# Kernel optimization log

Measured on AMD Instinct MI355X. Metric: run time of the kernel, lower is better.

Reference implementation:

```python
import jax, jax.numpy as jnp
import numpy as np

COMMITMENT_COST = 0.25
ENTROPY_WEIGHT = 0.1
EPS = 1e-10


def setup_inputs() -> dict:
    key = jax.random.key(0)
    k1, k2 = jax.random.split(key)
    B, L, D, K = 8, 4096, 256, 4096
    z = jax.random.normal(k1, (B, L, D), dtype=jnp.float32)
    # torch init: uniform(-1/K, 1/K)
    codebook_weight = jax.random.uniform(k2, (K, D), dtype=jnp.float32,
                                         minval=-1.0 / K, maxval=1.0 / K)
    return {"z": z, "codebook_weight": codebook_weight}


def reference(z, codebook_weight):
    B, L, D = z.shape
    z_flat = z.reshape(-1, D)                       # [N, D]
    # squared euclidean distances: [N, K]
    d2 = (jnp.sum(z_flat ** 2, axis=1, keepdims=True)
          + jnp.sum(codebook_weight ** 2, axis=1)
          - 2.0 * z_flat @ codebook_weight.T)
    indices = jnp.argmin(d2, axis=1)                # [N]
    z_q_flat = codebook_weight[indices]             # gather [N, D]
    z_q = z_q_flat.reshape(B, L, D)

    codebook_loss = jnp.mean((z_q - jax.lax.stop_gradient(z)) ** 2)
    commitment_loss = jnp.mean((jax.lax.stop_gradient(z_q) - z) ** 2)

    probs = jax.nn.softmax(-d2, axis=1)             # [N, K]
    avg_probs = probs.mean(axis=0)                  # [K]
    entropy = -jnp.sum(avg_probs * jnp.log(avg_probs + EPS))
    entropy_loss = -entropy

    codebook_commitment_loss = codebook_loss + COMMITMENT_COST * commitment_loss
    scaled_entropy_loss = ENTROPY_WEIGHT * entropy_loss
    vq_loss = codebook_commitment_loss + scaled_entropy_loss

    # straight-through estimator
    z_q_ste = z + jax.lax.stop_gradient(z_q - z)
    indices_out = indices.reshape(B, L)
    return (z_q_ste, indices_out, vq_loss, codebook_commitment_loss, scaled_entropy_loss)
```

## Files before the change

kernel.cpp:

```cpp
#include <hip/hip_runtime.h>
#include <stdint.h>

#define NROWS 32768
#define KC 4096
#define DIM 256
#define BM 64
#define TPS 64
#define CAP 40
#define KAPPA 0.99960f
#define K2L2E 2.88539008f
#define L2E 1.44269504f

#define OUT_IDX (NROWS * DIM)
#define OUT_SCAL (OUT_IDX + NROWS)

#define WS_CNORM 0
#define WS_ZNORM 16384
#define WS_LOSS  147456
#define WS_AVGP8 147712
#define WS_FRAG  278784

typedef __bf16 bf8 __attribute__((ext_vector_type(8)));
typedef float f16v __attribute__((ext_vector_type(16)));

#define GLOAD_LDS(g, l) \
  __builtin_amdgcn_global_load_lds( \
      (const __attribute__((address_space(1))) void*)(g), \
      (__attribute__((address_space(3))) void*)(l), 16, 0, 0)

__device__ __forceinline__ unsigned ford(float f) {
  unsigned u = __float_as_uint(f);
  return (u & 0x80000000u) ? ~u : (u | 0x80000000u);
}

__device__ __forceinline__ float np_rownorm256(const float* __restrict__ p) {
  float h[2];
  #pragma unroll
  for (int half = 0; half < 2; ++half) {
    const float* b = p + half * 128;
    float r[8];
    {
      float4 v0 = *(const float4*)(b);
      float4 v1 = *(const float4*)(b + 4);
      r[0] = __fmul_rn(v0.x, v0.x); r[1] = __fmul_rn(v0.y, v0.y);
      r[2] = __fmul_rn(v0.z, v0.z); r[3] = __fmul_rn(v0.w, v0.w);
      r[4] = __fmul_rn(v1.x, v1.x); r[5] = __fmul_rn(v1.y, v1.y);
      r[6] = __fmul_rn(v1.z, v1.z); r[7] = __fmul_rn(v1.w, v1.w);
    }
    for (int i = 8; i < 128; i += 8) {
      float4 v0 = *(const float4*)(b + i);
      float4 v1 = *(const float4*)(b + i + 4);
      r[0] = __fadd_rn(r[0], __fmul_rn(v0.x, v0.x));
      r[1] = __fadd_rn(r[1], __fmul_rn(v0.y, v0.y));
      r[2] = __fadd_rn(r[2], __fmul_rn(v0.z, v0.z));
      r[3] = __fadd_rn(r[3], __fmul_rn(v0.w, v0.w));
      r[4] = __fadd_rn(r[4], __fmul_rn(v1.x, v1.x));
      r[5] = __fadd_rn(r[5], __fmul_rn(v1.y, v1.y));
      r[6] = __fadd_rn(r[6], __fmul_rn(v1.z, v1.z));
      r[7] = __fadd_rn(r[7], __fmul_rn(v1.w, v1.w));
    }
    h[half] = __fadd_rn(
        __fadd_rn(__fadd_rn(r[0], r[1]), __fadd_rn(r[2], r[3])),
        __fadd_rn(__fadd_rn(r[4], r[5]), __fadd_rn(r[6], r[7])));
  }
  return __fadd_rn(h[0], h[1]);
}

__global__ void k_norms(const float* __restrict__ cbw, const float* __restrict__ z,
                        float* __restrict__ cnorm, float* __restrict__ znorm) {
  int r = blockIdx.x * 256 + threadIdx.x;
  if (r < KC) cnorm[r] = np_rownorm256(cbw + (size_t)r * DIM);
  else {
    int q = r - KC;
    if (q < NROWS) znorm[q] = np_rownorm256(z + (size_t)q * DIM);
  }
}

__global__ void k_frag(const float* __restrict__ cbw, __bf16* __restrict__ frag) {
  int idx = blockIdx.x * 256 + threadIdx.x;
  int c = idx >> 5, u = idx & 31;
  int ds = u >> 1, half = u & 1;
  int ct = c >> 5, m = c & 31;
  int lane = half * 32 + m;
  const float* src = cbw + (size_t)c * DIM + ds * 16 + half * 8;
  float4 a = *(const float4*)src;
  float4 b = *(const float4*)(src + 4);
  bf8 h;
  h[0] = (__bf16)a.x; h[1] = (__bf16)a.y; h[2] = (__bf16)a.z; h[3] = (__bf16)a.w;
  h[4] = (__bf16)b.x; h[5] = (__bf16)b.y; h[6] = (__bf16)b.z; h[7] = (__bf16)b.w;
  *(bf8*)(frag + ((size_t)(ct * 16 + ds) * 64 + lane) * 8) = h;
}

__device__ __forceinline__ float exact_d2(const float* __restrict__ zr,
                                          const float* __restrict__ cr,
                                          float rn, float cn) {
  float mm = 0.f;
  for (int d = 0; d < DIM; d += 4) {
    float4 zv = *(const float4*)(zr + d);
    float4 cv = *(const float4*)(cr + d);
    mm = __builtin_fmaf(zv.x, cv.x, mm);
    mm = __builtin_fmaf(zv.y, cv.y, mm);
    mm = __builtin_fmaf(zv.z, cv.z, mm);
    mm = __builtin_fmaf(zv.w, cv.w, mm);
  }
  return __fsub_rn(__fadd_rn(rn, cn), __fmul_rn(2.f, mm));
}

#define BLD(bs, c) (*(const bf8*)((bs) + (c) * 512 + lane * 8))

#define AQ_ALL(OP) OP(0) OP(1) OP(2) OP(3) OP(4) OP(5) OP(6) OP(7) \
                   OP(8) OP(9) OP(10) OP(11) OP(12) OP(13) OP(14) OP(15)
#define AQ_DECL(i) const bf8 aq##i = \
  *(const bf8*)&BstA[((size_t)(wr * 16 + (i)) * 64 + lane) * 8];

#define MF(A, B) acc = __builtin_amdgcn_mfma_f32_32x32x16_bf16((A), (B), acc, 0, 0, 0);
#define CONS16(bs_) { \
  __builtin_amdgcn_s_setprio(1); \
  MF(aq0,  BLD(bs_,0))  MF(aq1,  BLD(bs_,1))  MF(aq2,  BLD(bs_,2))  \
  MF(aq3,  BLD(bs_,3))  MF(aq4,  BLD(bs_,4))  MF(aq5,  BLD(bs_,5))  \
  MF(aq6,  BLD(bs_,6))  MF(aq7,  BLD(bs_,7))  MF(aq8,  BLD(bs_,8))  \
  MF(aq9,  BLD(bs_,9))  MF(aq10, BLD(bs_,10)) MF(aq11, BLD(bs_,11)) \
  MF(aq12, BLD(bs_,12)) MF(aq13, BLD(bs_,13)) MF(aq14, BLD(bs_,14)) \
  MF(aq15, BLD(bs_,15)) \
  __builtin_amdgcn_s_setprio(0); }

__global__ __launch_bounds__(256, 2) void k_main(
    const float* __restrict__ z, const float* __restrict__ cbw,
    const float* __restrict__ cnorm, const float* __restrict__ znorm,
    const __bf16* __restrict__ frag, float* __restrict__ out,
    float* __restrict__ avgp8, double* __restrict__ losssum) {
  __shared__ __attribute__((aligned(16))) __bf16 BstX[2][8192];
  __shared__ __attribute__((aligned(16))) __bf16 BstY[2][8192];
  __shared__ int cand[BM][CAP];
  __shared__ int ccount[BM];
  __shared__ unsigned rowmaxU[BM];
  __shared__ unsigned long long rowkey[BM];
  __shared__ float esumL[BM], invR[BM], lred[256];
  __shared__ int idxr[BM];

  const int t = threadIdx.x;
  const int lane = t & 63, wv = t >> 6;
  const int ln31 = lane & 31, lh = lane >> 5;
  const int wr = wv >> 1, wc = wv & 1;
  const int row0 = blockIdx.x * BM;
  const int ctbase = wc * TPS;

  if (t < BM) {
    ccount[t] = 0; rowmaxU[t] = 0u; rowkey[t] = ~0ULL; esumL[t] = 0.f;
  }

  __bf16* BstA = &BstX[0][0];
  #pragma unroll
  for (int i = 0; i < 8; ++i) {
    int idx = i * 256 + t;
    int l = idx & 63, ds = (idx >> 6) & 15, rt = idx >> 10;
    int row = rt * 32 + (l & 31), d0 = ds * 16 + (l >> 5) * 8;
    const float* src = z + (size_t)(row0 + row) * DIM + d0;
    float4 a = *(const float4*)src;
    float4 b = *(const float4*)(src + 4);
    bf8 h;
    h[0] = (__bf16)a.x; h[1] = (__bf16)a.y; h[2] = (__bf16)a.z; h[3] = (__bf16)a.w;
    h[4] = (__bf16)b.x; h[5] = (__bf16)b.y; h[6] = (__bf16)b.z; h[7] = (__bf16)b.w;
    *(bf8*)&BstA[((size_t)((rt * 16 + ds) * 64 + l)) * 8] = h;
  }
  __syncthreads();

  AQ_ALL(AQ_DECL)
  __syncthreads();

  #define STG_A(ARR, ct) { \
    const char* g_ = (const char*)frag + (size_t)(ct) * 16384 + wr * 8192 \
                     + (size_t)lane * 16; \
    char* l_ = (char*)(&ARR[wc][0]) + wr * 8192; \
    GLOAD_LDS(g_, l_);               GLOAD_LDS(g_ + 1024, l_ + 1024); \
    GLOAD_LDS(g_ + 2048, l_ + 2048); GLOAD_LDS(g_ + 3072, l_ + 3072); \
    GLOAD_LDS(g_ + 4096, l_ + 4096); GLOAD_LDS(g_ + 5120, l_ + 5120); \
    GLOAD_LDS(g_ + 6144, l_ + 6144); GLOAD_LDS(g_ + 7168, l_ + 7168); \
  }

  float es[16];
  #pragma unroll
  for (int i = 0; i < 16; ++i) es[i] = 0.f;

  #define PRIME_EPI(ctv) { \
    const float cnl = cnorm[(ctv) * 32 + ln31] * L2E; \
    _Pragma("unroll") \
    for (int r = 0; r < 16; ++r) { \
      const int row = wr * 32 + (r & 3) + 8 * (r >> 2) + 4 * lh; \
      float e = exp2f(__builtin_fmaf(acc[r], K2L2E, -cnl)); \
      atomicMax(&rowmaxU[row], __float_as_uint(e));   \
    } \
  }

  #define SWEEP_EPI(ctv) { \
    const float cnl = cnorm[(ctv) * 32 + ln31] * L2E; \
    float cr[16]; \
    { \
      const float4* rmf = (const float4*)(rowmaxU + wr * 32); \
      float4 c0 = rmf[lh], c1 = rmf[2 + lh], c2 = rmf[4 + lh], c3 = rmf[6 + lh]; \
      cr[0]  = c0.x; cr[1]  = c0.y; cr[2]  = c0.z; cr[3]  = c0.w; \
      cr[4]  = c1.x; cr[5]  = c1.y; cr[6]  = c1.z; cr[7]  = c1.w; \
      cr[8]  = c2.x; cr[9]  = c2.y; cr[10] = c2.z; cr[11] = c2.w; \
      cr[12] = c3.x; cr[13] = c3.y; cr[14] = c3.z; cr[15] = c3.w; \
    } \
    unsigned cond = 0u; \
    _Pragma("unroll") \
    for (int r = 0; r < 16; ++r) { \
      float e = exp2f(__builtin_fmaf(acc[r], K2L2E, -cnl)); \
      es[r] += e;                        \
      cond |= (e >= cr[r] * KAPPA) ? (1u << r) : 0u; \
    } \
    if (cond) {    \
      _Pragma("unroll") \
      for (int r = 0; r < 16; ++r) { \
        if (cond & (1u << r)) { \
          const int row = wr * 32 + (r & 3) + 8 * (r >> 2) + 4 * lh; \
          float e = exp2f(__builtin_fmaf(acc[r], K2L2E, -cnl)); \
          atomicMax(&rowmaxU[row], __float_as_uint(e)); \
          int slot = atomicAdd(&ccount[row], 1); \
          if (slot < CAP) cand[row][slot] = (ctv) * 32 + ln31; \
        } \
      } \
    } \
  }

  #define P1BODY(RDARR, WRARR, ctv, ctn, EPI) { \
    STG_A(WRARR, (ctn)) \
    f16v acc; \
    _Pragma("unroll") \
    for (int r = 0; r < 16; ++r) acc[r] = 0.f; \
    CONS16((const __bf16*)&RDARR[wc][0]) \
    EPI((ctv)) \
    __syncthreads(); \
  }

  {
    STG_A(BstX, ctbase)
    __syncthreads();
    P1BODY(BstX, BstY, ctbase, ctbase, PRIME_EPI)
    for (int p = 0; p < 32; ++p) {
      const int i1 = 2 * p + 1, i2 = 2 * p + 2;
      P1BODY(BstY, BstX, ctbase + i1 - 1, ctbase + i1, SWEEP_EPI)
      {
        const int nx = (i2 < 64) ? ctbase + i2 : ctbase + 63;
        P1BODY(BstX, BstY, ctbase + i2 - 1, nx, SWEEP_EPI)
      }
    }
  }

  #pragma unroll
  for (int r = 0; r < 16; ++r) {
    float e = es[r];
    #pragma unroll
    for (int off = 16; off > 0; off >>= 1) e += __shfl_xor(e, off);
    if (ln31 == 0) {
      const int row = wr * 32 + (r & 3) + 8 * (r >> 2) + 4 * lh;
      atomicAdd(&esumL[row], e);
    }
  }
  __syncthreads();
  if (t < BM) invR[t] = 1.0f / esumL[t];
  __syncthreads();

  {
    int r = t & 63, q = t >> 6;
    int cnt = ccount[r];
    const float* zr = z + (size_t)(row0 + r) * DIM;
    float rn = znorm[row0 + r];
    if (cnt <= CAP) {
      for (int s = q; s < cnt; s += 4) {
        int k = cand[r][s];
        float d2 = exact_d2(zr, cbw + (size_t)k * DIM, rn, cnorm[k]);
        atomicMin(&rowkey[r], (((unsigned long long)ford(d2)) << 32) | (unsigned)k);
      }
    } else {
      for (int k = q; k < KC; k += 4) {
        float d2 = exact_d2(zr, cbw + (size_t)k * DIM, rn, cnorm[k]);
        atomicMin(&rowkey[r], (((unsigned long long)ford(d2)) << 32) | (unsigned)k);
      }
    }
  }
  __syncthreads();
  if (t < BM) {
    int idx = (int)(rowkey[t] & 0xFFFFFFFFULL);
    idxr[t] = idx;
    out[OUT_IDX + row0 + t] = (float)idx;
  }
  __syncthreads();

  float lacc = 0.f;
  for (int r = 0; r < BM; ++r) {
    int idx = idxr[r];
    float zq = cbw[(size_t)idx * DIM + t];
    float zv = z[(size_t)(row0 + r) * DIM + t];
    float df = __fsub_rn(zq, zv);
    out[(size_t)(row0 + r) * DIM + t] = __fadd_rn(zv, df);
    lacc += df * df;
  }
  lred[t] = lacc;
  __syncthreads();
  #pragma unroll
  for (int s = 128; s > 0; s >>= 1) {
    if (t < s) lred[t] += lred[t + s];
    __syncthreads();
  }
  if (t == 0) atomicAdd(losssum, (double)lred[0]);

  float ir[16];
  #pragma unroll
  for (int r = 0; r < 16; ++r)
    ir[r] = invR[wr * 32 + (r & 3) + 8 * (r >> 2) + 4 * lh];
  __syncthreads();

  #define P2EPI(ctv) { \
    const float cnl = cnorm[(ctv) * 32 + ln31] * L2E; \
    float s2 = 0.f; \
    _Pragma("unroll") \
    for (int r = 0; r < 16; ++r) { \
      float e = exp2f(__builtin_fmaf(acc[r], K2L2E, -cnl)); \
      s2 = __builtin_fmaf(e, ir[r], s2); \
    } \
    s2 += __shfl_xor(s2, 32);            \
    if (lh == 0) atomicAdd(&shadow[(ctv) * 32 + ln31], s2); \
  }

  {
    float* shadow = avgp8 + (size_t)(blockIdx.x & 7) * KC;
    STG_A(BstX, ctbase)
    __syncthreads();
    for (int p = 0; p < 32; ++p) {
      const int i0 = 2 * p, i1 = 2 * p + 1;
      P1BODY(BstX, BstY, ctbase + i0, ctbase + i1, P2EPI)
      {
        const int nx = (i1 + 1 < 64) ? ctbase + i1 + 1 : ctbase + 63;
        P1BODY(BstY, BstX, ctbase + i1, nx, P2EPI)
      }
    }
  }
}

__global__ void k_final(const float* __restrict__ avgp8,
                        const double* __restrict__ losssum,
                        float* __restrict__ out) {
  const int t = threadIdx.x;
  double part = 0.0;
  for (int k = t; k < KC; k += 256) {
    float a4 = 0.f;
    #pragma unroll
    for (int s = 0; s < 8; ++s) a4 += avgp8[s * KC + k];
    double a = (double)a4 / (double)NROWS;
    part += a * log(a + 1e-10);
  }
  __shared__ double sd[256];
  sd[t] = part;
  __syncthreads();
  for (int s = 128; s > 0; s >>= 1) {
    if (t < s) sd[t] += sd[t + s];
    __syncthreads();
  }
  if (t == 0) {
    double H = -sd[0];
    double mse = losssum[0] / (double)((size_t)NROWS * DIM);
    double ccl = 1.25 * mse;
    double sel = -0.1 * H;
    out[OUT_SCAL + 0] = (float)(ccl + sel);
    out[OUT_SCAL + 1] = (float)ccl;
    out[OUT_SCAL + 2] = (float)sel;
  }
}

extern "C" void kernel_launch(void* const* d_in, const int* in_sizes, int n_in,
                              void* d_out, int out_size, void* d_ws, size_t ws_size,
                              hipStream_t stream) {
  const float* z = (const float*)d_in[0];
  const float* cbw = (const float*)d_in[1];
  float* out = (float*)d_out;
  char* ws = (char*)d_ws;
  float* cnorm = (float*)(ws + WS_CNORM);
  float* znorm = (float*)(ws + WS_ZNORM);
  double* losssum = (double*)(ws + WS_LOSS);
  float* avgp8 = (float*)(ws + WS_AVGP8);
  __bf16* frag = (__bf16*)(ws + WS_FRAG);

  hipMemsetAsync(ws + WS_LOSS, 0, 8, stream);
  hipMemsetAsync(ws + WS_AVGP8, 0, 8 * KC * 4, stream);
  k_norms<<<(KC + NROWS) / 256, 256, 0, stream>>>(cbw, z, cnorm, znorm);
  k_frag<<<(KC * 32) / 256, 256, 0, stream>>>(cbw, frag);
  k_main<<<NROWS / BM, 256, 0, stream>>>(z, cbw, cnorm, znorm, frag, out,
                                         avgp8, losssum);
  k_final<<<1, 256, 0, stream>>>(avgp8, losssum, out);
}
```

Before: 397.2 us.

## Software-pipeline MFMA and epilogue with two accumulator sets in both sweeps

Adds a second accumulator so each step issues the MFMA chain for tile i+1 before running the exp/atomic epilogue for tile i. This overlaps the transcendental epilogue work with matrix-core execution in both the candidate sweep and the softmax-average sweep. In exchange it needs more registers, which may pressure occupancy at launch bounds of 2 blocks per CU. The buffer-staging order is reworked to match the deeper pipeline.

New measurement: 399.8 us. No clear change (+0.7%).

```diff
diff --git a/kernel.cpp b/kernel.cpp
--- a/kernel.cpp
+++ b/kernel.cpp
@@ -113,16 +113,21 @@
 #define AQ_DECL(i) const bf8 aq##i = \
   *(const bf8*)&BstA[((size_t)(wr * 16 + (i)) * 64 + lane) * 8];
 
-#define MF(A, B) acc = __builtin_amdgcn_mfma_f32_32x32x16_bf16((A), (B), acc, 0, 0, 0);
-#define CONS16(bs_) { \
+#define MF2(ACC, A, B) ACC = __builtin_amdgcn_mfma_f32_32x32x16_bf16((A), (B), ACC, 0, 0, 0);
+#define CONS16(ACC, bs_) { \
   __builtin_amdgcn_s_setprio(1); \
-  MF(aq0,  BLD(bs_,0))  MF(aq1,  BLD(bs_,1))  MF(aq2,  BLD(bs_,2))  \
-  MF(aq3,  BLD(bs_,3))  MF(aq4,  BLD(bs_,4))  MF(aq5,  BLD(bs_,5))  \
-  MF(aq6,  BLD(bs_,6))  MF(aq7,  BLD(bs_,7))  MF(aq8,  BLD(bs_,8))  \
-  MF(aq9,  BLD(bs_,9))  MF(aq10, BLD(bs_,10)) MF(aq11, BLD(bs_,11)) \
-  MF(aq12, BLD(bs_,12)) MF(aq13, BLD(bs_,13)) MF(aq14, BLD(bs_,14)) \
-  MF(aq15, BLD(bs_,15)) \
+  MF2(ACC, aq0,  BLD(bs_,0))  MF2(ACC, aq1,  BLD(bs_,1))  \
+  MF2(ACC, aq2,  BLD(bs_,2))  MF2(ACC, aq3,  BLD(bs_,3))  \
+  MF2(ACC, aq4,  BLD(bs_,4))  MF2(ACC, aq5,  BLD(bs_,5))  \
+  MF2(ACC, aq6,  BLD(bs_,6))  MF2(ACC, aq7,  BLD(bs_,7))  \
+  MF2(ACC, aq8,  BLD(bs_,8))  MF2(ACC, aq9,  BLD(bs_,9))  \
+  MF2(ACC, aq10, BLD(bs_,10)) MF2(ACC, aq11, BLD(bs_,11)) \
+  MF2(ACC, aq12, BLD(bs_,12)) MF2(ACC, aq13, BLD(bs_,13)) \
+  MF2(ACC, aq14, BLD(bs_,14)) MF2(ACC, aq15, BLD(bs_,15)) \
   __builtin_amdgcn_s_setprio(0); }
+
+#define ZERO16(ACC) { _Pragma("unroll") \
+  for (int r_ = 0; r_ < 16; ++r_) ACC[r_] = 0.f; }
 
 __global__ __launch_bounds__(256, 2) void k_main(
     const float* __restrict__ z, const float* __restrict__ cbw,
@@ -177,22 +182,24 @@
     GLOAD_LDS(g_ + 4096, l_ + 4096); GLOAD_LDS(g_ + 5120, l_ + 5120); \
     GLOAD_LDS(g_ + 6144, l_ + 6144); GLOAD_LDS(g_ + 7168, l_ + 7168); \
   }
+  #define XP ((const __bf16*)&BstX[wc][0])
+  #define YP ((const __bf16*)&BstY[wc][0])
 
   float es[16];
   #pragma unroll
   for (int i = 0; i < 16; ++i) es[i] = 0.f;
 
-  #define PRIME_EPI(ctv) { \
+  #define PRIME_EPI(ACC, ctv) { \
     const float cnl = cnorm[(ctv) * 32 + ln31] * L2E; \
     _Pragma("unroll") \
     for (int r = 0; r < 16; ++r) { \
       const int row = wr * 32 + (r & 3) + 8 * (r >> 2) + 4 * lh; \
-      float e = exp2f(__builtin_fmaf(acc[r], K2L2E, -cnl)); \
+      float e = exp2f(__builtin_fmaf(ACC[r], K2L2E, -cnl)); \
       atomicMax(&rowmaxU[row], __float_as_uint(e));   \
     } \
   }
 
-  #define SWEEP_EPI(ctv) { \
+  #define SWEEP_EPI(ACC, ctv) { \
     const float cnl = cnorm[(ctv) * 32 + ln31] * L2E; \
     float cr[16]; \
     { \
@@ -206,7 +213,7 @@
     unsigned cond = 0u; \
     _Pragma("unroll") \
     for (int r = 0; r < 16; ++r) { \
-      float e = exp2f(__builtin_fmaf(acc[r], K2L2E, -cnl)); \
+      float e = exp2f(__builtin_fmaf(ACC[r], K2L2E, -cnl)); \
       es[r] += e;                        \
       cond |= (e >= cr[r] * KAPPA) ? (1u << r) : 0u; \
     } \
@@ -215,7 +222,7 @@
       for (int r = 0; r < 16; ++r) { \
         if (cond & (1u << r)) { \
           const int row = wr * 32 + (r & 3) + 8 * (r >> 2) + 4 * lh; \
-          float e = exp2f(__builtin_fmaf(acc[r], K2L2E, -cnl)); \
+          float e = exp2f(__builtin_fmaf(ACC[r], K2L2E, -cnl)); \
           atomicMax(&rowmaxU[row], __float_as_uint(e)); \
           int slot = atomicAdd(&ccount[row], 1); \
           if (slot < CAP) cand[row][slot] = (ctv) * 32 + ln31; \
@@ -224,28 +231,35 @@
     } \
   }
 
-  #define P1BODY(RDARR, WRARR, ctv, ctn, EPI) { \
-    STG_A(WRARR, (ctn)) \
-    f16v acc; \
-    _Pragma("unroll") \
-    for (int r = 0; r < 16; ++r) acc[r] = 0.f; \
-    CONS16((const __bf16*)&RDARR[wc][0]) \
-    EPI((ctv)) \
-    __syncthreads(); \
-  }
-
   {
+    f16v accU, accV;
     STG_A(BstX, ctbase)
     __syncthreads();
-    P1BODY(BstX, BstY, ctbase, ctbase, PRIME_EPI)
-    for (int p = 0; p < 32; ++p) {
-      const int i1 = 2 * p + 1, i2 = 2 * p + 2;
-      P1BODY(BstY, BstX, ctbase + i1 - 1, ctbase + i1, SWEEP_EPI)
+    STG_A(BstY, ctbase)
+    ZERO16(accU) CONS16(accU, XP)
+    __syncthreads();
+    STG_A(BstX, ctbase + 1)
+    ZERO16(accV) CONS16(accV, YP)
+    PRIME_EPI(accU, ctbase)
+    __syncthreads();
+    STG_A(BstY, ctbase + 2)
+    ZERO16(accU) CONS16(accU, XP)
+    SWEEP_EPI(accV, ctbase)
+    __syncthreads();
+    for (int p = 1; p < 32; ++p) {
+      STG_A(BstX, ctbase + 2 * p + 1)
+      ZERO16(accV) CONS16(accV, YP)
+      SWEEP_EPI(accU, ctbase + 2 * p - 1)
+      __syncthreads();
       {
-        const int nx = (i2 < 64) ? ctbase + i2 : ctbase + 63;
-        P1BODY(BstX, BstY, ctbase + i2 - 1, nx, SWEEP_EPI)
+        const int nx = (2 * p + 2 <= 63) ? (ctbase + 2 * p + 2) : (ctbase + 63);
+        STG_A(BstY, nx)
       }
-    }
+      ZERO16(accU) CONS16(accU, XP)
+      SWEEP_EPI(accV, ctbase + 2 * p)
+      __syncthreads();
+    }
+    SWEEP_EPI(accU, ctbase + 63)
   }
 
   #pragma unroll
@@ -312,12 +326,12 @@
     ir[r] = invR[wr * 32 + (r & 3) + 8 * (r >> 2) + 4 * lh];
   __syncthreads();
 
-  #define P2EPI(ctv) { \
+  #define P2EPI(ACC, ctv) { \
     const float cnl = cnorm[(ctv) * 32 + ln31] * L2E; \
     float s2 = 0.f; \
     _Pragma("unroll") \
     for (int r = 0; r < 16; ++r) { \
-      float e = exp2f(__builtin_fmaf(acc[r], K2L2E, -cnl)); \
+      float e = exp2f(__builtin_fmaf(ACC[r], K2L2E, -cnl)); \
       s2 = __builtin_fmaf(e, ir[r], s2); \
     } \
     s2 += __shfl_xor(s2, 32);            \
@@ -326,16 +340,25 @@
 
   {
     float* shadow = avgp8 + (size_t)(blockIdx.x & 7) * KC;
+    f16v accU, accV;
     STG_A(BstX, ctbase)
     __syncthreads();
-    for (int p = 0; p < 32; ++p) {
-      const int i0 = 2 * p, i1 = 2 * p + 1;
-      P1BODY(BstX, BstY, ctbase + i0, ctbase + i1, P2EPI)
-      {
-        const int nx = (i1 + 1 < 64) ? ctbase + i1 + 1 : ctbase + 63;
-        P1BODY(BstY, BstX, ctbase + i1, nx, P2EPI)
-      }
-    }
+    STG_A(BstY, ctbase + 1)
+    ZERO16(accU) CONS16(accU, XP)
+    __syncthreads();
+    for (int p = 0; p < 31; ++p) {
+      STG_A(BstX, ctbase + 2 * p + 2)
+      ZERO16(accV) CONS16(accV, YP)
+      P2EPI(accU, ctbase + 2 * p)
+      __syncthreads();
+      STG_A(BstY, ctbase + 2 * p + 3)
+      ZERO16(accU) CONS16(accU, XP)
+      P2EPI(accV, ctbase + 2 * p + 1)
+      __syncthreads();
+    }
+    ZERO16(accV) CONS16(accV, YP)
+    P2EPI(accU, ctbase + 62)
+    P2EPI(accV, ctbase + 63)
   }
 }
 
```

## Fuse prep kernels and memsets, compute z row norms inside main kernel

Applied to the files above, without the earlier changes.

Merges the codebook-norm and bf16 fragment-packing kernels plus the two workspace memsets into one prep launch. The z row norms are now computed inside the main kernel from rows each block already loads, so they are no longer written to and re-read from global memory. This removes three launches and a full pass over z, at the cost of 64 threads per main block doing a serial 256-element norm before the first barrier.

Result: faster. 387.2 us (-2.5%).

```diff
diff --git a/kernel.cpp b/kernel.cpp
--- a/kernel.cpp
+++ b/kernel.cpp
@@ -66,29 +66,32 @@
   return __fadd_rn(h[0], h[1]);
 }
 
-__global__ void k_norms(const float* __restrict__ cbw, const float* __restrict__ z,
-                        float* __restrict__ cnorm, float* __restrict__ znorm) {
-  int r = blockIdx.x * 256 + threadIdx.x;
-  if (r < KC) cnorm[r] = np_rownorm256(cbw + (size_t)r * DIM);
-  else {
-    int q = r - KC;
-    if (q < NROWS) znorm[q] = np_rownorm256(z + (size_t)q * DIM);
-  }
-}
-
-__global__ void k_frag(const float* __restrict__ cbw, __bf16* __restrict__ frag) {
-  int idx = blockIdx.x * 256 + threadIdx.x;
-  int c = idx >> 5, u = idx & 31;
-  int ds = u >> 1, half = u & 1;
-  int ct = c >> 5, m = c & 31;
-  int lane = half * 32 + m;
-  const float* src = cbw + (size_t)c * DIM + ds * 16 + half * 8;
-  float4 a = *(const float4*)src;
-  float4 b = *(const float4*)(src + 4);
-  bf8 h;
-  h[0] = (__bf16)a.x; h[1] = (__bf16)a.y; h[2] = (__bf16)a.z; h[3] = (__bf16)a.w;
-  h[4] = (__bf16)b.x; h[5] = (__bf16)b.y; h[6] = (__bf16)b.z; h[7] = (__bf16)b.w;
-  *(bf8*)(frag + ((size_t)(ct * 16 + ds) * 64 + lane) * 8) = h;
+__global__ void k_prep(const float* __restrict__ cbw, __bf16* __restrict__ frag,
+                       float* __restrict__ cnorm, float* __restrict__ avgp8,
+                       double* __restrict__ losssum) {
+  const int b = blockIdx.x;
+  if (b < 512) {
+    int idx = b * 256 + threadIdx.x;
+    int c = idx >> 5, u = idx & 31;
+    int ds = u >> 1, half = u & 1;
+    int ct = c >> 5, m = c & 31;
+    int lane = half * 32 + m;
+    const float* src = cbw + (size_t)c * DIM + ds * 16 + half * 8;
+    float4 a = *(const float4*)src;
+    float4 bb = *(const float4*)(src + 4);
+    bf8 h;
+    h[0] = (__bf16)a.x;  h[1] = (__bf16)a.y;  h[2] = (__bf16)a.z;  h[3] = (__bf16)a.w;
+    h[4] = (__bf16)bb.x; h[5] = (__bf16)bb.y; h[6] = (__bf16)bb.z; h[7] = (__bf16)bb.w;
+    *(bf8*)(frag + ((size_t)(ct * 16 + ds) * 64 + lane) * 8) = h;
+  } else {
+    const int q = b - 512;
+    int r = q * 256 + threadIdx.x;
+    cnorm[r] = np_rownorm256(cbw + (size_t)r * DIM);
+    float* ap = avgp8 + (size_t)q * 2048 + threadIdx.x;
+    #pragma unroll
+    for (int i = 0; i < 8; ++i) ap[i * 256] = 0.f;
+    if (q == 0 && threadIdx.x == 0) *losssum = 0.0;
+  }
 }
 
 __device__ __forceinline__ float exact_d2(const float* __restrict__ zr,
@@ -126,7 +129,7 @@
 
 __global__ __launch_bounds__(256, 2) void k_main(
     const float* __restrict__ z, const float* __restrict__ cbw,
-    const float* __restrict__ cnorm, const float* __restrict__ znorm,
+    const float* __restrict__ cnorm,
     const __bf16* __restrict__ frag, float* __restrict__ out,
     float* __restrict__ avgp8, double* __restrict__ losssum) {
   __shared__ __attribute__((aligned(16))) __bf16 BstX[2][8192];
@@ -136,6 +139,7 @@
   __shared__ unsigned rowmaxU[BM];
   __shared__ unsigned long long rowkey[BM];
   __shared__ float esumL[BM], invR[BM], lred[256];
+  __shared__ float znormL[BM];
   __shared__ int idxr[BM];
 
   const int t = threadIdx.x;
@@ -163,6 +167,7 @@
     h[4] = (__bf16)b.x; h[5] = (__bf16)b.y; h[6] = (__bf16)b.z; h[7] = (__bf16)b.w;
     *(bf8*)&BstA[((size_t)((rt * 16 + ds) * 64 + l)) * 8] = h;
   }
+  if (t < BM) znormL[t] = np_rownorm256(z + (size_t)(row0 + t) * DIM);
   __syncthreads();
 
   AQ_ALL(AQ_DECL)
@@ -266,7 +271,7 @@
     int r = t & 63, q = t >> 6;
     int cnt = ccount[r];
     const float* zr = z + (size_t)(row0 + r) * DIM;
-    float rn = znorm[row0 + r];
+    float rn = znormL[r];
     if (cnt <= CAP) {
       for (int s = q; s < cnt; s += 4) {
         int k = cand[r][s];
@@ -377,16 +382,12 @@
   float* out = (float*)d_out;
   char* ws = (char*)d_ws;
   float* cnorm = (float*)(ws + WS_CNORM);
-  float* znorm = (float*)(ws + WS_ZNORM);
   double* losssum = (double*)(ws + WS_LOSS);
   float* avgp8 = (float*)(ws + WS_AVGP8);
   __bf16* frag = (__bf16*)(ws + WS_FRAG);
 
-  hipMemsetAsync(ws + WS_LOSS, 0, 8, stream);
-  hipMemsetAsync(ws + WS_AVGP8, 0, 8 * KC * 4, stream);
-  k_norms<<<(KC + NROWS) / 256, 256, 0, stream>>>(cbw, z, cnorm, znorm);
-  k_frag<<<(KC * 32) / 256, 256, 0, stream>>>(cbw, frag);
-  k_main<<<NROWS / BM, 256, 0, stream>>>(z, cbw, cnorm, znorm, frag, out,
+  k_prep<<<528, 256, 0, stream>>>(cbw, frag, cnorm, avgp8, losssum);
+  k_main<<<NROWS / BM, 256, 0, stream>>>(z, cbw, cnorm, frag, out,
                                          avgp8, losssum);
   k_final<<<1, 256, 0, stream>>>(avgp8, losssum, out);
 }
```
